# Kernel tuning notes

Measured on AMD Instinct MI355X. Metric: run time of the kernel, lower is better.

The kernel has to match this reference:

```python
import jax, jax.numpy as jnp
import numpy as np

NUM_HEADS = 8
HIDDEN_DIM = 256
QUERY_DIM = 256
HEAD_DIM = HIDDEN_DIM // NUM_HEADS
NORM_FACT = float(HIDDEN_DIM / NUM_HEADS) ** (-0.5)


def setup_inputs() -> dict:
    key = jax.random.key(0)
    k1, k2, k3, k4, k5 = jax.random.split(key, 5)
    B, Q, H, W = 16, 100, 64, 64
    q = jax.random.normal(k1, (B, Q, QUERY_DIM), dtype=jnp.float32)
    k = jax.random.normal(k2, (B, QUERY_DIM, H, W), dtype=jnp.float32)
    mask = jax.random.randint(k3, (B, H, W), 0, 2).astype(jnp.bool_)
    # xavier_uniform for [hidden, query] linear weights
    limit = float(np.sqrt(6.0 / (HIDDEN_DIM + QUERY_DIM)))
    Wq = jax.random.uniform(k4, (HIDDEN_DIM, QUERY_DIM), minval=-limit, maxval=limit, dtype=jnp.float32)
    Wk = jax.random.uniform(k5, (HIDDEN_DIM, QUERY_DIM), minval=-limit, maxval=limit, dtype=jnp.float32)
    bq = jnp.zeros((HIDDEN_DIM,), dtype=jnp.float32)
    bk = jnp.zeros((HIDDEN_DIM,), dtype=jnp.float32)
    return {"q": q, "k": k, "Wq": Wq, "bq": bq, "Wk": Wk, "bk": bk, "mask": mask}


def reference(q, k, Wq, bq, Wk, bk, mask):
    B, Q, _ = q.shape
    _, C, H, W = k.shape
    # q projection: [B, Q, hidden]
    qp = jnp.einsum('bqc,hc->bqh', q, Wq) + bq
    # k projection via 1x1 conv == channelwise linear: [B, hidden, H, W]
    kp = jnp.einsum('bchw,oc->bohw', k, Wk) + bk[None, :, None, None]
    # split heads: qh [B,Q,nh,hd], kh [B,nh,hd,H,W]
    qh = qp.reshape(B, Q, NUM_HEADS, HEAD_DIM)
    kh = kp.reshape(B, NUM_HEADS, HEAD_DIM, H, W)
    # scores [B,Q,nh,H,W]
    weights = jnp.einsum('bqnd,bndhw->bqnhw', qh, kh) * NORM_FACT
    # masked fill: mask [B,H,W] -> broadcast over (Q, heads)
    weights = jnp.where(mask[:, None, None, :, :], -jnp.inf, weights)
    # softmax jointly over (heads, H, W), as in torch flatten(2)
    flat = weights.reshape(B, Q, NUM_HEADS * H * W)
    flat = jax.nn.softmax(flat, axis=-1)
    return flat.reshape(B, Q, NUM_HEADS, H, W)
```

## Files before the change

### kernel.cpp

```cpp
#include <hip/hip_runtime.h>
#include <hip/hip_bf16.h>
#include <math.h>

#define BB 16
#define QQ 100
#define NH 8
#define HWN 4096
#define NORM_FACT 0.17677669529663687f
#define QPAD 112

#define KPF_IDX(b, tile, n, kg) (((((size_t)(b) * 256 + (tile)) * 8 + (n)) * 4 + (kg)) * 128)

typedef short bf16x8_t __attribute__((ext_vector_type(8)));
typedef float f32x4_t  __attribute__((ext_vector_type(4)));

__device__ __forceinline__ unsigned short bf16bits(float f) {
    __hip_bfloat16 h = __float2bfloat16(f);
    return __builtin_bit_cast(unsigned short, h);
}
__device__ __forceinline__ float bf16tof(unsigned short u) {
    union { unsigned int i; float f; } x; x.i = (unsigned int)u << 16; return x.f;
}

__global__ void k_prep(const float* __restrict__ Wq, const float* __restrict__ Wk,
                       float* __restrict__ WqT, unsigned short* __restrict__ Wkbf) {
    int idx = blockIdx.x;
    int h = threadIdx.x;
    if (idx < 256) {
        WqT[idx * 256 + h] = Wq[h * 256 + idx];
    } else {
        int r = idx - 256;
        Wkbf[r * 256 + h] = bf16bits(Wk[r * 256 + h]);
    }
}

__global__ __launch_bounds__(256) void k_qproj(const float* __restrict__ q,
                                               const float* __restrict__ WqT,
                                               const float* __restrict__ bq,
                                               unsigned short* __restrict__ qphi,
                                               unsigned short* __restrict__ qplo) {
    int blk = blockIdx.x;
    int b = blk / 28, q0 = (blk % 28) * 4;
    int h = threadIdx.x;
    size_t obase = ((size_t)b * QPAD + q0) * 256 + h;
    if (q0 >= QQ) {
#pragma unroll
        for (int i = 0; i < 4; ++i) { qphi[obase + i * 256] = 0; qplo[obase + i * 256] = 0; }
        return;
    }
    __shared__ float qsh[4][256];
    int ibase = (b * QQ + q0) * 256;
#pragma unroll
    for (int i = 0; i < 4; ++i) qsh[i][h] = q[ibase + i * 256 + h];
    __syncthreads();
    float bias = bq[h];
    float a0 = bias, a1 = bias, a2 = bias, a3 = bias;
    for (int c = 0; c < 256; ++c) {
        float wv = WqT[c * 256 + h];
        a0 = fmaf(qsh[0][c], wv, a0);
        a1 = fmaf(qsh[1][c], wv, a1);
        a2 = fmaf(qsh[2][c], wv, a2);
        a3 = fmaf(qsh[3][c], wv, a3);
    }
    float a[4] = {a0 * NORM_FACT, a1 * NORM_FACT, a2 * NORM_FACT, a3 * NORM_FACT};
#pragma unroll
    for (int i = 0; i < 4; ++i) {
        unsigned short hi = bf16bits(a[i]);
        qphi[obase + i * 256] = hi;
        qplo[obase + i * 256] = bf16bits(a[i] - bf16tof(hi));
    }
}

__global__ __launch_bounds__(512) void k_kproj4(const float* __restrict__ k,
                                                const unsigned short* __restrict__ Wkbf,
                                                const float* __restrict__ bk,
                                                unsigned short* __restrict__ kpf) {
    int b = blockIdx.y;
    int hwblk = blockIdx.x * 64;
    int t = threadIdx.x;
    int w = t >> 6, lane = t & 63;
    int hwt = w & 3, oh = w >> 2;
    int n15 = lane & 15, kg = lane >> 4;
    int hw_l = hwt * 16 + n15;

    __shared__ float lds_f[64][68];

    f32x4_t acc[8];
#pragma unroll
    for (int m = 0; m < 8; ++m) acc[m] = f32x4_t{0.f, 0.f, 0.f, 0.f};

    const float* kb = k + (size_t)b * 256 * HWN + hwblk;
    const unsigned short* wbase = Wkbf + ((size_t)(oh * 128 + n15)) * 256 + kg * 8;
    int c_l = t >> 4, l16 = t & 15;

#pragma unroll 1
    for (int chunk = 0; chunk < 4; ++chunk) {
#pragma unroll
        for (int p = 0; p < 2; ++p) {
            int cc = p * 32 + c_l;
            float4 v = *(const float4*)(kb + (size_t)(chunk * 64 + cc) * HWN + l16 * 4);
            lds_f[l16 * 4 + 0][cc] = v.x;
            lds_f[l16 * 4 + 1][cc] = v.y;
            lds_f[l16 * 4 + 2][cc] = v.z;
            lds_f[l16 * 4 + 3][cc] = v.w;
        }
        __syncthreads();
#pragma unroll
        for (int ksl = 0; ksl < 2; ++ksl) {
            f32x4_t f0 = *(const f32x4_t*)&lds_f[hw_l][ksl * 32 + kg * 8];
            f32x4_t f1 = *(const f32x4_t*)&lds_f[hw_l][ksl * 32 + kg * 8 + 4];
            bf16x8_t bfrag;
#pragma unroll
            for (int j = 0; j < 4; ++j) {
                bfrag[j]     = (short)bf16bits(f0[j]);
                bfrag[4 + j] = (short)bf16bits(f1[j]);
            }
            int ks = chunk * 2 + ksl;
#pragma unroll
            for (int m = 0; m < 8; ++m) {
                bf16x8_t afrag = *reinterpret_cast<const bf16x8_t*>(wbase + (size_t)m * 16 * 256 + ks * 32);
                acc[m] = __builtin_amdgcn_mfma_f32_16x16x32_bf16(afrag, bfrag, acc[m], 0, 0, 0);
            }
        }
        __syncthreads();
    }

    unsigned short* tile2 = (unsigned short*)lds_f;
#pragma unroll 1
    for (int ohp = 0; ohp < 2; ++ohp) {
        if (oh == ohp) {
#pragma unroll
            for (int m = 0; m < 8; ++m) {
                ushort4 pk;
                unsigned short* pkp = (unsigned short*)&pk;
#pragma unroll
                for (int r = 0; r < 4; ++r) {
                    int o = ohp * 128 + m * 16 + kg * 4 + r;
                    pkp[r] = bf16bits(acc[m][r] + bk[o]);
                }
                *(ushort4*)&tile2[(size_t)hw_l * 132 + m * 16 + kg * 4] = pk;
            }
        }
        __syncthreads();
        {
            int s = t * 2;
            int tile = s >> 8;
            int n2   = (s >> 6) & 3;
            int kgc  = (s >> 4) & 3;
            int nl   = s & 15;
            const unsigned short* src = &tile2[(size_t)(tile * 16 + nl) * 132 + n2 * 32 + kgc * 8];
            uint4 v0 = *(const uint4*)(src);
            uint4 v1 = *(const uint4*)(src + 132);
            size_t dst = KPF_IDX(b, blockIdx.x * 4 + tile, ohp * 4 + n2, kgc) + nl * 8;
            *(uint4*)(kpf + dst)     = v0;
            *(uint4*)(kpf + dst + 8) = v1;
        }
        __syncthreads();
    }
}

__global__ __launch_bounds__(256) void k_sums(const unsigned short* __restrict__ qphi,
                                              const unsigned short* __restrict__ qplo,
                                              const unsigned short* __restrict__ kpf,
                                              const int* __restrict__ mask,
                                              float* __restrict__ partial) {
    int hwb = blockIdx.x, b = blockIdx.y;
    int t = threadIdx.x, w = t >> 6, lane = t & 63;
    int n15 = lane & 15, kg = lane >> 4;
    int hw = hwb * 64 + w * 16 + n15;
    float mm = mask[b * HWN + hw] ? 0.0f : 1.0f;

    __shared__ float ldsbuf[8960];
    unsigned short* sA = (unsigned short*)ldsbuf;

    int tg = hwb * 4 + w;
    bf16x8_t bfr[8];
#pragma unroll
    for (int n = 0; n < NH; ++n)
        bfr[n] = *reinterpret_cast<const bf16x8_t*>(kpf + KPF_IDX(b, tg, n, kg) + n15 * 8);

    const unsigned short* ghi = qphi + (size_t)b * QPAD * 256;
    const unsigned short* glo = qplo + (size_t)b * QPAD * 256;
    int srow = t >> 4, schunk = t & 15;

    float sums[7][4] = {};
#pragma unroll 1
    for (int mt = 0; mt < 7; ++mt) {
        const unsigned short* shi = ghi + (size_t)(mt * 16 + srow) * 256 + schunk * 16;
        const unsigned short* slo = glo + (size_t)(mt * 16 + srow) * 256 + schunk * 16;
        uint4 vhi0 = *(const uint4*)(shi);
        uint4 vhi1 = *(const uint4*)(shi + 8);
        uint4 vlo0 = *(const uint4*)(slo);
        uint4 vlo1 = *(const uint4*)(slo + 8);
        *(uint4*)&sA[srow * 264 + schunk * 16]          = vhi0;
        *(uint4*)&sA[srow * 264 + schunk * 16 + 8]      = vhi1;
        *(uint4*)&sA[16 * 264 + srow * 264 + schunk * 16]     = vlo0;
        *(uint4*)&sA[16 * 264 + srow * 264 + schunk * 16 + 8] = vlo1;
        __syncthreads();
#pragma unroll
        for (int n = 0; n < NH; ++n) {
            bf16x8_t ahi = *reinterpret_cast<const bf16x8_t*>(&sA[n15 * 264 + n * 32 + kg * 8]);
            bf16x8_t alo = *reinterpret_cast<const bf16x8_t*>(&sA[16 * 264 + n15 * 264 + n * 32 + kg * 8]);
            f32x4_t a2 = {0.f, 0.f, 0.f, 0.f};
            a2 = __builtin_amdgcn_mfma_f32_16x16x32_bf16(ahi, bfr[n], a2, 0, 0, 0);
            a2 = __builtin_amdgcn_mfma_f32_16x16x32_bf16(alo, bfr[n], a2, 0, 0, 0);
#pragma unroll
            for (int r = 0; r < 4; ++r)
                sums[mt][r] += __expf(a2[r]) * mm;
        }
        __syncthreads();
    }

    float* R = ldsbuf + w * 112 * 20;
#pragma unroll
    for (int mt = 0; mt < 7; ++mt)
#pragma unroll
        for (int r = 0; r < 4; ++r)
            R[(mt * 16 + kg * 4 + r) * 20 + n15] = sums[mt][r];
    if (lane < 56) {
#pragma unroll
        for (int p = 0; p < 2; ++p) {
            int row = lane + p * 56;
            f32x4_t v0 = *(const f32x4_t*)&R[row * 20 + 0];
            f32x4_t v1 = *(const f32x4_t*)&R[row * 20 + 4];
            f32x4_t v2 = *(const f32x4_t*)&R[row * 20 + 8];
            f32x4_t v3 = *(const f32x4_t*)&R[row * 20 + 12];
            float s = (v0[0]+v0[1]+v0[2]+v0[3]) + (v1[0]+v1[1]+v1[2]+v1[3])
                    + (v2[0]+v2[1]+v2[2]+v2[3]) + (v3[0]+v3[1]+v3[2]+v3[3]);
            partial[((size_t)b * QPAD + row) * 256 + hwb * 4 + w] = s;
        }
    }
}

__global__ __launch_bounds__(256) void k_invsum(const float* __restrict__ partial,
                                                float* __restrict__ inv) {
    int blk = blockIdx.x;
    int b = blk / QQ, qq = blk % QQ;
    const float* p = partial + ((size_t)b * QPAD + qq) * 256;
    int t = threadIdx.x;
    float v = p[t];
#pragma unroll
    for (int off = 32; off; off >>= 1) v += __shfl_xor(v, off, 64);
    __shared__ float red[4];
    if ((t & 63) == 0) red[t >> 6] = v;
    __syncthreads();
    if (t == 0) inv[blk] = 1.0f / (red[0] + red[1] + red[2] + red[3]);
}

__global__ __launch_bounds__(256) void k_write(const unsigned short* __restrict__ qphi,
                                               const unsigned short* __restrict__ qplo,
                                               const unsigned short* __restrict__ kpf,
                                               const int* __restrict__ mask,
                                               const float* __restrict__ inv,
                                               float* __restrict__ out) {
    int qt = blockIdx.x, n = blockIdx.y, b = blockIdx.z;
    int t = threadIdx.x, w = t >> 6, lane = t & 63;
    int n15 = lane & 15, kg = lane >> 4;

    bf16x8_t ahi = *reinterpret_cast<const bf16x8_t*>(
        qphi + ((size_t)(b * QPAD + qt * 16 + n15)) * 256 + n * 32 + kg * 8);
    bf16x8_t alo = *reinterpret_cast<const bf16x8_t*>(
        qplo + ((size_t)(b * QPAD + qt * 16 + n15)) * 256 + n * 32 + kg * 8);
    float invq[4];
#pragma unroll
    for (int r = 0; r < 4; ++r) {
        int qrow = qt * 16 + kg * 4 + r;
        invq[r] = (qrow < QQ) ? inv[b * QQ + qrow] : 0.0f;
    }

    __shared__ float lt[16][260];

    bf16x8_t bc[4], bn[4];
    float mc[4], mn[4];
#pragma unroll
    for (int ht = 0; ht < 4; ++ht) {
        int tg = w * 4 + ht;
        bc[ht] = *reinterpret_cast<const bf16x8_t*>(kpf + KPF_IDX(b, tg, n, kg) + n15 * 8);
        mc[ht] = mask[b * HWN + w * 64 + ht * 16 + n15] ? 0.0f : 1.0f;
        bn[ht] = bc[ht];
        mn[ht] = mc[ht];
    }

#pragma unroll 1
    for (int hws = 0; hws < 16; ++hws) {
        if (hws < 15) {
#pragma unroll
            for (int ht = 0; ht < 4; ++ht) {
                int tg = (hws + 1) * 16 + w * 4 + ht;
                bn[ht] = *reinterpret_cast<const bf16x8_t*>(kpf + KPF_IDX(b, tg, n, kg) + n15 * 8);
                mn[ht] = mask[b * HWN + (hws + 1) * 256 + w * 64 + ht * 16 + n15] ? 0.0f : 1.0f;
            }
        }
#pragma unroll
        for (int ht = 0; ht < 4; ++ht) {
            f32x4_t acc = {0.f, 0.f, 0.f, 0.f};
            acc = __builtin_amdgcn_mfma_f32_16x16x32_bf16(ahi, bc[ht], acc, 0, 0, 0);
            acc = __builtin_amdgcn_mfma_f32_16x16x32_bf16(alo, bc[ht], acc, 0, 0, 0);
#pragma unroll
            for (int r = 0; r < 4; ++r)
                lt[kg * 4 + r][w * 64 + ht * 16 + n15] = __expf(acc[r]) * mc[ht] * invq[r];
        }
        __syncthreads();
#pragma unroll
        for (int j = 0; j < 4; ++j) {
            int row = w * 4 + j;
            int qrow = qt * 16 + row;
            f32x4_t v4 = *(const f32x4_t*)&lt[row][lane * 4];
            if (qrow < QQ)
                __builtin_nontemporal_store(v4,
                    (f32x4_t*)(out + (((size_t)(b * QQ + qrow)) * NH + n) * HWN + hws * 256 + lane * 4));
        }
        __syncthreads();
#pragma unroll
        for (int ht = 0; ht < 4; ++ht) { bc[ht] = bn[ht]; mc[ht] = mn[ht]; }
    }
}

extern "C" void kernel_launch(void* const* d_in, const int* in_sizes, int n_in,
                              void* d_out, int out_size, void* d_ws, size_t ws_size,
                              hipStream_t stream) {
    const float* q    = (const float*)d_in[0];
    const float* k    = (const float*)d_in[1];
    const float* Wq   = (const float*)d_in[2];
    const float* bq   = (const float*)d_in[3];
    const float* Wk   = (const float*)d_in[4];
    const float* bk   = (const float*)d_in[5];
    const int*   mask = (const int*)d_in[6];
    float* out = (float*)d_out;

    char* base = (char*)d_ws;
    unsigned short* kpf  = (unsigned short*)(base);
    unsigned short* qphi = (unsigned short*)(base + 33554432);
    unsigned short* qplo = (unsigned short*)(base + 34471936);
    float*  WqT     = (float*)(base + 35389440);
    unsigned short* Wkbf = (unsigned short*)(base + 35651584);
    float*  partial = (float*)(base + 35782656);
    float*  inv     = (float*)(base + 37617664);
    if (ws_size < (size_t)37624064) return;

    k_prep  <<<dim3(512), dim3(256), 0, stream>>>(Wq, Wk, WqT, Wkbf);
    k_qproj <<<dim3(448), dim3(256), 0, stream>>>(q, WqT, bq, qphi, qplo);
    k_kproj4<<<dim3(64, 16), dim3(512), 0, stream>>>(k, Wkbf, bk, kpf);
    k_sums  <<<dim3(64, 16), dim3(256), 0, stream>>>(qphi, qplo, kpf, mask, partial);
    k_invsum<<<dim3(1600), dim3(256), 0, stream>>>(partial, inv);
    k_write <<<dim3(7, 8, 16), dim3(256), 0, stream>>>(qphi, qplo, kpf, mask, inv, out);
}
```

Baseline: 186.5 us.

## Double-buffer LDS in kproj and write kernels, split write grid over HW halves

In k_kproj4, global loads for the next channel chunk are prefetched into registers and written into alternating LDS buffers, which removes one barrier per chunk. Its epilogue writes both output halves to a single wider LDS tile and stores it in one pass. k_write now splits the HW range across twice as many blocks, double-buffers its LDS staging tile to drop the trailing barrier, and uses plain stores instead of nontemporal ones. The aim is more parallelism and fewer syncs in the output-write phase, at the cost of extra LDS and a reliance on alternating buffers being safe with a single barrier per iteration.

```diff
diff --git a/kernel.cpp b/kernel.cpp
--- a/kernel.cpp
+++ b/kernel.cpp
@@ -83,7 +83,7 @@
     int n15 = lane & 15, kg = lane >> 4;
     int hw_l = hwt * 16 + n15;
 
-    __shared__ float lds_f[64][68];
+    __shared__ float ldsbuf[8704];
 
     f32x4_t acc[8];
 #pragma unroll
@@ -93,22 +93,29 @@
     const unsigned short* wbase = Wkbf + ((size_t)(oh * 128 + n15)) * 256 + kg * 8;
     int c_l = t >> 4, l16 = t & 15;
 
+    float4 r0 = *(const float4*)(kb + (size_t)(c_l) * HWN + l16 * 4);
+    float4 r1 = *(const float4*)(kb + (size_t)(32 + c_l) * HWN + l16 * 4);
+
 #pragma unroll 1
     for (int chunk = 0; chunk < 4; ++chunk) {
-#pragma unroll
-        for (int p = 0; p < 2; ++p) {
-            int cc = p * 32 + c_l;
-            float4 v = *(const float4*)(kb + (size_t)(chunk * 64 + cc) * HWN + l16 * 4);
-            lds_f[l16 * 4 + 0][cc] = v.x;
-            lds_f[l16 * 4 + 1][cc] = v.y;
-            lds_f[l16 * 4 + 2][cc] = v.z;
-            lds_f[l16 * 4 + 3][cc] = v.w;
+        float* sbuf = ldsbuf + (chunk & 1) * 4352;
+        sbuf[(l16 * 4 + 0) * 68 + c_l] = r0.x;
+        sbuf[(l16 * 4 + 1) * 68 + c_l] = r0.y;
+        sbuf[(l16 * 4 + 2) * 68 + c_l] = r0.z;
+        sbuf[(l16 * 4 + 3) * 68 + c_l] = r0.w;
+        sbuf[(l16 * 4 + 0) * 68 + 32 + c_l] = r1.x;
+        sbuf[(l16 * 4 + 1) * 68 + 32 + c_l] = r1.y;
+        sbuf[(l16 * 4 + 2) * 68 + 32 + c_l] = r1.z;
+        sbuf[(l16 * 4 + 3) * 68 + 32 + c_l] = r1.w;
+        if (chunk < 3) {
+            r0 = *(const float4*)(kb + (size_t)((chunk + 1) * 64 + c_l) * HWN + l16 * 4);
+            r1 = *(const float4*)(kb + (size_t)((chunk + 1) * 64 + 32 + c_l) * HWN + l16 * 4);
         }
         __syncthreads();
 #pragma unroll
         for (int ksl = 0; ksl < 2; ++ksl) {
-            f32x4_t f0 = *(const f32x4_t*)&lds_f[hw_l][ksl * 32 + kg * 8];
-            f32x4_t f1 = *(const f32x4_t*)&lds_f[hw_l][ksl * 32 + kg * 8 + 4];
+            f32x4_t f0 = *(const f32x4_t*)&sbuf[hw_l * 68 + ksl * 32 + kg * 8];
+            f32x4_t f1 = *(const f32x4_t*)&sbuf[hw_l * 68 + ksl * 32 + kg * 8 + 4];
             bf16x8_t bfrag;
 #pragma unroll
             for (int j = 0; j < 4; ++j) {
@@ -122,40 +129,32 @@
                 acc[m] = __builtin_amdgcn_mfma_f32_16x16x32_bf16(afrag, bfrag, acc[m], 0, 0, 0);
             }
         }
-        __syncthreads();
-    }
-
-    unsigned short* tile2 = (unsigned short*)lds_f;
-#pragma unroll 1
-    for (int ohp = 0; ohp < 2; ++ohp) {
-        if (oh == ohp) {
-#pragma unroll
-            for (int m = 0; m < 8; ++m) {
-                ushort4 pk;
-                unsigned short* pkp = (unsigned short*)&pk;
-#pragma unroll
-                for (int r = 0; r < 4; ++r) {
-                    int o = ohp * 128 + m * 16 + kg * 4 + r;
-                    pkp[r] = bf16bits(acc[m][r] + bk[o]);
-                }
-                *(ushort4*)&tile2[(size_t)hw_l * 132 + m * 16 + kg * 4] = pk;
-            }
-        }
-        __syncthreads();
-        {
-            int s = t * 2;
-            int tile = s >> 8;
-            int n2   = (s >> 6) & 3;
-            int kgc  = (s >> 4) & 3;
-            int nl   = s & 15;
-            const unsigned short* src = &tile2[(size_t)(tile * 16 + nl) * 132 + n2 * 32 + kgc * 8];
-            uint4 v0 = *(const uint4*)(src);
-            uint4 v1 = *(const uint4*)(src + 132);
-            size_t dst = KPF_IDX(b, blockIdx.x * 4 + tile, ohp * 4 + n2, kgc) + nl * 8;
-            *(uint4*)(kpf + dst)     = v0;
-            *(uint4*)(kpf + dst + 8) = v1;
-        }
-        __syncthreads();
+    }
+    __syncthreads();
+
+    unsigned short* tile2 = (unsigned short*)ldsbuf;
+#pragma unroll
+    for (int m = 0; m < 8; ++m) {
+        ushort4 pk;
+        unsigned short* pkp = (unsigned short*)&pk;
+#pragma unroll
+        for (int r = 0; r < 4; ++r) {
+            int o = oh * 128 + m * 16 + kg * 4 + r;
+            pkp[r] = bf16bits(acc[m][r] + bk[o]);
+        }
+        *(ushort4*)&tile2[(size_t)hw_l * 264 + oh * 128 + m * 16 + kg * 4] = pk;
+    }
+    __syncthreads();
+#pragma unroll
+    for (int i = 0; i < 4; ++i) {
+        int s = i * 512 + t;
+        int n15c = s & 15;
+        int kgc  = (s >> 4) & 3;
+        int nc   = (s >> 6) & 7;
+        int tile = (s >> 9) & 3;
+        const unsigned short* src = &tile2[(size_t)(tile * 16 + n15c) * 264 + nc * 32 + kgc * 8];
+        size_t dst = KPF_IDX(b, blockIdx.x * 4 + tile, nc, kgc) + n15c * 8;
+        *(uint4*)(kpf + dst) = *(const uint4*)src;
     }
 }
 
@@ -253,9 +252,12 @@
                                                const int* __restrict__ mask,
                                                const float* __restrict__ inv,
                                                float* __restrict__ out) {
-    int qt = blockIdx.x, n = blockIdx.y, b = blockIdx.z;
+    int bx = blockIdx.x;
+    int qt = bx % 7, half = bx / 7;
+    int n = blockIdx.y, b = blockIdx.z;
     int t = threadIdx.x, w = t >> 6, lane = t & 63;
     int n15 = lane & 15, kg = lane >> 4;
+    int hws0 = half * 8;
 
     bf16x8_t ahi = *reinterpret_cast<const bf16x8_t*>(
         qphi + ((size_t)(b * QPAD + qt * 16 + n15)) * 256 + n * 32 + kg * 8);
@@ -268,22 +270,24 @@
         invq[r] = (qrow < QQ) ? inv[b * QQ + qrow] : 0.0f;
     }
 
-    __shared__ float lt[16][260];
+    __shared__ float lt[2][16][260];
 
     bf16x8_t bc[4], bn[4];
     float mc[4], mn[4];
 #pragma unroll
     for (int ht = 0; ht < 4; ++ht) {
-        int tg = w * 4 + ht;
+        int tg = hws0 * 16 + w * 4 + ht;
         bc[ht] = *reinterpret_cast<const bf16x8_t*>(kpf + KPF_IDX(b, tg, n, kg) + n15 * 8);
-        mc[ht] = mask[b * HWN + w * 64 + ht * 16 + n15] ? 0.0f : 1.0f;
+        mc[ht] = mask[b * HWN + hws0 * 256 + w * 64 + ht * 16 + n15] ? 0.0f : 1.0f;
         bn[ht] = bc[ht];
         mn[ht] = mc[ht];
     }
 
 #pragma unroll 1
-    for (int hws = 0; hws < 16; ++hws) {
-        if (hws < 15) {
+    for (int i = 0; i < 8; ++i) {
+        int hws = hws0 + i;
+        int buf = i & 1;
+        if (i < 7) {
 #pragma unroll
             for (int ht = 0; ht < 4; ++ht) {
                 int tg = (hws + 1) * 16 + w * 4 + ht;
@@ -298,19 +302,17 @@
             acc = __builtin_amdgcn_mfma_f32_16x16x32_bf16(alo, bc[ht], acc, 0, 0, 0);
 #pragma unroll
             for (int r = 0; r < 4; ++r)
-                lt[kg * 4 + r][w * 64 + ht * 16 + n15] = __expf(acc[r]) * mc[ht] * invq[r];
+                lt[buf][kg * 4 + r][w * 64 + ht * 16 + n15] = __expf(acc[r]) * mc[ht] * invq[r];
         }
         __syncthreads();
 #pragma unroll
         for (int j = 0; j < 4; ++j) {
             int row = w * 4 + j;
             int qrow = qt * 16 + row;
-            f32x4_t v4 = *(const f32x4_t*)&lt[row][lane * 4];
+            f32x4_t v4 = *(const f32x4_t*)&lt[buf][row][lane * 4];
             if (qrow < QQ)
-                __builtin_nontemporal_store(v4,
-                    (f32x4_t*)(out + (((size_t)(b * QQ + qrow)) * NH + n) * HWN + hws * 256 + lane * 4));
-        }
-        __syncthreads();
+                *(f32x4_t*)(out + (((size_t)(b * QQ + qrow)) * NH + n) * HWN + hws * 256 + lane * 4) = v4;
+        }
 #pragma unroll
         for (int ht = 0; ht < 4; ++ht) { bc[ht] = bn[ht]; mc[ht] = mn[ht]; }
     }
@@ -343,5 +345,5 @@
     k_kproj4<<<dim3(64, 16), dim3(512), 0, stream>>>(k, Wkbf, bk, kpf);
     k_sums  <<<dim3(64, 16), dim3(256), 0, stream>>>(qphi, qplo, kpf, mask, partial);
     k_invsum<<<dim3(1600), dim3(256), 0, stream>>>(partial, inv);
-    k_write <<<dim3(7, 8, 16), dim3(256), 0, stream>>>(qphi, qplo, kpf, mask, inv, out);
-}
+    k_write <<<dim3(14, 8, 16), dim3(256), 0, stream>>>(qphi, qplo, kpf, mask, inv, out);
+}
```

Result: no change. 189.4 us (+1.5%).

## Prefetch all k-projection input into registers and write output in one pass

Applied to the files above, without the earlier changes.

The k-projection kernel now issues all eight global loads per thread up front into registers, then stages them to LDS in two halves instead of four load-sync chunks, so the loads overlap with the conversion and MFMA work. The epilogue writes both output-head halves into a wider LDS tile at once and stores with one barrier, removing the serialized two-pass writeback. This raises register and LDS use per block (a 64x133 float tile), which may reduce occupancy.

```diff
diff --git a/kernel.cpp b/kernel.cpp
--- a/kernel.cpp
+++ b/kernel.cpp
@@ -71,7 +71,7 @@
     }
 }
 
-__global__ __launch_bounds__(512) void k_kproj4(const float* __restrict__ k,
+__global__ __launch_bounds__(512) void k_kproj5(const float* __restrict__ k,
                                                 const unsigned short* __restrict__ Wkbf,
                                                 const float* __restrict__ bk,
                                                 unsigned short* __restrict__ kpf) {
@@ -83,39 +83,44 @@
     int n15 = lane & 15, kg = lane >> 4;
     int hw_l = hwt * 16 + n15;
 
-    __shared__ float lds_f[64][68];
-
-    f32x4_t acc[8];
-#pragma unroll
-    for (int m = 0; m < 8; ++m) acc[m] = f32x4_t{0.f, 0.f, 0.f, 0.f};
+    __shared__ float lds_f[64 * 133];
 
     const float* kb = k + (size_t)b * 256 * HWN + hwblk;
     const unsigned short* wbase = Wkbf + ((size_t)(oh * 128 + n15)) * 256 + kg * 8;
     int c_l = t >> 4, l16 = t & 15;
 
+    float4 rg[8];
+#pragma unroll
+    for (int p = 0; p < 8; ++p)
+        rg[p] = *(const float4*)(kb + (size_t)(p * 32 + c_l) * HWN + l16 * 4);
+
+    f32x4_t acc[8];
+#pragma unroll
+    for (int m = 0; m < 8; ++m) acc[m] = f32x4_t{0.f, 0.f, 0.f, 0.f};
+
 #pragma unroll 1
-    for (int chunk = 0; chunk < 4; ++chunk) {
-#pragma unroll
-        for (int p = 0; p < 2; ++p) {
+    for (int half = 0; half < 2; ++half) {
+#pragma unroll
+        for (int p = 0; p < 4; ++p) {
+            float4 v = rg[half * 4 + p];
             int cc = p * 32 + c_l;
-            float4 v = *(const float4*)(kb + (size_t)(chunk * 64 + cc) * HWN + l16 * 4);
-            lds_f[l16 * 4 + 0][cc] = v.x;
-            lds_f[l16 * 4 + 1][cc] = v.y;
-            lds_f[l16 * 4 + 2][cc] = v.z;
-            lds_f[l16 * 4 + 3][cc] = v.w;
-        }
-        __syncthreads();
-#pragma unroll
-        for (int ksl = 0; ksl < 2; ++ksl) {
-            f32x4_t f0 = *(const f32x4_t*)&lds_f[hw_l][ksl * 32 + kg * 8];
-            f32x4_t f1 = *(const f32x4_t*)&lds_f[hw_l][ksl * 32 + kg * 8 + 4];
+            lds_f[(l16 * 4 + 0) * 133 + cc] = v.x;
+            lds_f[(l16 * 4 + 1) * 133 + cc] = v.y;
+            lds_f[(l16 * 4 + 2) * 133 + cc] = v.z;
+            lds_f[(l16 * 4 + 3) * 133 + cc] = v.w;
+        }
+        __syncthreads();
+#pragma unroll
+        for (int ksl = 0; ksl < 4; ++ksl) {
+            f32x4_t f0 = *(const f32x4_t*)&lds_f[hw_l * 133 + ksl * 32 + kg * 8];
+            f32x4_t f1 = *(const f32x4_t*)&lds_f[hw_l * 133 + ksl * 32 + kg * 8 + 4];
             bf16x8_t bfrag;
 #pragma unroll
             for (int j = 0; j < 4; ++j) {
                 bfrag[j]     = (short)bf16bits(f0[j]);
                 bfrag[4 + j] = (short)bf16bits(f1[j]);
             }
-            int ks = chunk * 2 + ksl;
+            int ks = half * 4 + ksl;
 #pragma unroll
             for (int m = 0; m < 8; ++m) {
                 bf16x8_t afrag = *reinterpret_cast<const bf16x8_t*>(wbase + (size_t)m * 16 * 256 + ks * 32);
@@ -126,36 +131,28 @@
     }
 
     unsigned short* tile2 = (unsigned short*)lds_f;
-#pragma unroll 1
-    for (int ohp = 0; ohp < 2; ++ohp) {
-        if (oh == ohp) {
-#pragma unroll
-            for (int m = 0; m < 8; ++m) {
-                ushort4 pk;
-                unsigned short* pkp = (unsigned short*)&pk;
-#pragma unroll
-                for (int r = 0; r < 4; ++r) {
-                    int o = ohp * 128 + m * 16 + kg * 4 + r;
-                    pkp[r] = bf16bits(acc[m][r] + bk[o]);
-                }
-                *(ushort4*)&tile2[(size_t)hw_l * 132 + m * 16 + kg * 4] = pk;
-            }
-        }
-        __syncthreads();
-        {
-            int s = t * 2;
-            int tile = s >> 8;
-            int n2   = (s >> 6) & 3;
-            int kgc  = (s >> 4) & 3;
-            int nl   = s & 15;
-            const unsigned short* src = &tile2[(size_t)(tile * 16 + nl) * 132 + n2 * 32 + kgc * 8];
-            uint4 v0 = *(const uint4*)(src);
-            uint4 v1 = *(const uint4*)(src + 132);
-            size_t dst = KPF_IDX(b, blockIdx.x * 4 + tile, ohp * 4 + n2, kgc) + nl * 8;
-            *(uint4*)(kpf + dst)     = v0;
-            *(uint4*)(kpf + dst + 8) = v1;
-        }
-        __syncthreads();
+#pragma unroll
+    for (int m = 0; m < 8; ++m) {
+        ushort4 pk;
+        unsigned short* pkp = (unsigned short*)&pk;
+#pragma unroll
+        for (int r = 0; r < 4; ++r) {
+            int o = oh * 128 + m * 16 + kg * 4 + r;
+            pkp[r] = bf16bits(acc[m][r] + bk[o]);
+        }
+        *(ushort4*)&tile2[(size_t)hw_l * 266 + oh * 128 + m * 16 + kg * 4] = pk;
+    }
+    __syncthreads();
+#pragma unroll
+    for (int i = 0; i < 4; ++i) {
+        int s = i * 512 + t;
+        int n15c = s & 15;
+        int kgc  = (s >> 4) & 3;
+        int nc   = (s >> 6) & 7;
+        int tile = (s >> 9) & 3;
+        const unsigned short* src = &tile2[(size_t)(tile * 16 + n15c) * 266 + nc * 32 + kgc * 8];
+        size_t dst = KPF_IDX(b, blockIdx.x * 4 + tile, nc, kgc) + n15c * 8;
+        *(uint4*)(kpf + dst) = *(const uint4*)src;
     }
 }
 
@@ -340,7 +337,7 @@
 
     k_prep  <<<dim3(512), dim3(256), 0, stream>>>(Wq, Wk, WqT, Wkbf);
     k_qproj <<<dim3(448), dim3(256), 0, stream>>>(q, WqT, bq, qphi, qplo);
-    k_kproj4<<<dim3(64, 16), dim3(512), 0, stream>>>(k, Wkbf, bk, kpf);
+    k_kproj5<<<dim3(64, 16), dim3(512), 0, stream>>>(k, Wkbf, bk, kpf);
     k_sums  <<<dim3(64, 16), dim3(256), 0, stream>>>(qphi, qplo, kpf, mask, partial);
     k_invsum<<<dim3(1600), dim3(256), 0, stream>>>(partial, inv);
     k_write <<<dim3(7, 8, 16), dim3(256), 0, stream>>>(qphi, qplo, kpf, mask, inv, out);
```

New measurement: 202.8 us. 8.7% more time.
